# Performance work log

Hardware: AMD Instinct MI355X
Metric: run time of the kernel (lower is better)

Reference implementation:

```python
import jax, jax.numpy as jnp
import numpy as np

N = 8192
NUM_CLASSES = 20
IOU_THRESH = 0.5
IMAGE_SIZE = 1024.0
MAX_DELTA = 16.0


def setup_inputs() -> dict:
    key = jax.random.key(0)
    k1, k2, k3, k4 = jax.random.split(key, 4)
    deltas = jax.random.uniform(k1, (N, 4), dtype=jnp.float32) * MAX_DELTA
    locations = jax.random.uniform(k2, (N, 2), dtype=jnp.float32) * IMAGE_SIZE
    scores = jax.random.uniform(k3, (N,), dtype=jnp.float32)
    class_ids = jax.random.randint(k4, (N,), 0, NUM_CLASSES, dtype=jnp.int32)
    return {"deltas": deltas, "locations": locations, "scores": scores,
            "class_ids": class_ids, "stride": 8}


def _apply_deltas_to_locations(deltas, locations, stride):
    # Faithful to fcos_apply_deltas_to_locations: clamp deltas at 0, then LTRB decode.
    d = jnp.clip(deltas, 0.0, None)
    xc, yc = locations[:, 0], locations[:, 1]
    s = jnp.asarray(stride, deltas.dtype)
    return jnp.stack([xc - d[:, 0] * s,
                      yc - d[:, 1] * s,
                      xc + d[:, 2] * s,
                      yc + d[:, 3] * s], axis=1)  # (N, 4) x1,y1,x2,y2


def _class_spec_nms(boxes, scores, class_ids, iou_threshold):
    # Class-offset trick (same math as class_spec_nms): shift boxes per class so
    # boxes of different classes never overlap.
    max_coord = jnp.max(boxes)
    offsets = class_ids.astype(boxes.dtype) * (max_coord + 1.0)
    b = boxes + offsets[:, None]

    # Sort by descending score (greedy order of the sequential python loop).
    order = jnp.argsort(-scores)
    bs = b[order]
    x1, y1, x2, y2 = bs[:, 0], bs[:, 1], bs[:, 2], bs[:, 3]
    areas = (x2 - x1) * (y2 - y1)

    # Pairwise IoU in sorted order -- the parallel-bitmask form of the
    # sequential suppression (exactly the same IoU math as `nms`).
    xx1 = jnp.maximum(x1[:, None], x1[None, :])
    yy1 = jnp.maximum(y1[:, None], y1[None, :])
    xx2 = jnp.minimum(x2[:, None], x2[None, :])
    yy2 = jnp.minimum(y2[:, None], y2[None, :])
    inter = jnp.clip(xx2 - xx1, 0.0, None) * jnp.clip(yy2 - yy1, 0.0, None)
    union = areas[:, None] + areas[None, :] - inter
    iou = inter / union  # (N, N), no eps, matching the original

    n = boxes.shape[0]
    idx = jnp.arange(n)

    def body(i, keep):
        # Box i suppresses later boxes with IoU > threshold, only if i itself survives.
        sup = keep[i] & (iou[i] > iou_threshold) & (idx > i)
        return keep & ~sup

    keep_sorted = jax.lax.fori_loop(0, n, body, jnp.ones((n,), dtype=bool))
    # Boolean keep mask in ORIGINAL box order (fixed-shape stand-in for the
    # variable-length index list the torch version returns).
    keep_mask = jnp.zeros((n,), dtype=bool).at[order].set(keep_sorted)
    return keep_mask


def reference(deltas, locations, scores, class_ids, stride):
    boxes = _apply_deltas_to_locations(deltas, locations, stride)
    keep_mask = _class_spec_nms(boxes, scores, class_ids, IOU_THRESH)
    return boxes, keep_mask
```

## Files before the change

### kernel.cpp

```cpp
#include <hip/hip_runtime.h>
#include <stdint.h>

#define N 8192
#define NCLS 20
#define IOU_THRESH 0.5f
#define MAXC 576
#define NW 9

typedef unsigned long long u64;

#define WS_BLOCKMAX 0
#define WS_MAXC1    256
#define WS_ORDER    512
#define WS_X1S      33280
#define WS_Y1S      66048
#define WS_X2S      98816
#define WS_Y2S      131584
#define WS_AREAS    164352
#define WS_CLSLIST  197632
#define WS_CLSSTART 230400

__global__ __launch_bounds__(256) void k_boxes(const float* __restrict__ deltas,
                                               const float* __restrict__ loc,
                                               const int* __restrict__ stridep,
                                               float* __restrict__ outBoxes,
                                               float* __restrict__ blockmax) {
    int i = blockIdx.x * blockDim.x + threadIdx.x;
    int iv = stridep[0];
    float sf = (iv >= 0 && iv < (1 << 23)) ? (float)iv : __int_as_float(iv);

    float4 d = ((const float4*)deltas)[i];
    float2 c = ((const float2*)loc)[i];
    float d0 = fmaxf(d.x, 0.0f), d1 = fmaxf(d.y, 0.0f);
    float d2 = fmaxf(d.z, 0.0f), d3 = fmaxf(d.w, 0.0f);
    float p0 = d0 * sf, p1 = d1 * sf, p2 = d2 * sf, p3 = d3 * sf;
    asm volatile("" : "+v"(p0), "+v"(p1), "+v"(p2), "+v"(p3));
    float x1 = c.x - p0, y1 = c.y - p1, x2 = c.x + p2, y2 = c.y + p3;
    float4 b; b.x = x1; b.y = y1; b.z = x2; b.w = y2;
    ((float4*)outBoxes)[i] = b;

    float m = fmaxf(fmaxf(x1, y1), fmaxf(x2, y2));
    for (int off = 32; off; off >>= 1) m = fmaxf(m, __shfl_down(m, off));
    __shared__ float sm[4];
    int wid = threadIdx.x >> 6;
    if ((threadIdx.x & 63) == 0) sm[wid] = m;
    __syncthreads();
    if (threadIdx.x == 0)
        blockmax[blockIdx.x] = fmaxf(fmaxf(sm[0], sm[1]), fmaxf(sm[2], sm[3]));
}

__global__ __launch_bounds__(64) void k_maxreduce(const float* __restrict__ blockmax,
                                                  float* __restrict__ maxc1, int nb) {
    int l = threadIdx.x;
    float m = (l < nb) ? blockmax[l] : -1e38f;
    for (int off = 32; off; off >>= 1) m = fmaxf(m, __shfl_down(m, off));
    if (l == 0) maxc1[0] = m + 1.0f;
}

__global__ __launch_bounds__(1024) void k_sort(const float* __restrict__ scores,
                                               const int* __restrict__ cls,
                                               const float* __restrict__ boxes,
                                               const float* __restrict__ maxc1p,
                                               int* __restrict__ order,
                                               float* __restrict__ x1s, float* __restrict__ y1s,
                                               float* __restrict__ x2s, float* __restrict__ y2s,
                                               float* __restrict__ areas) {
    __shared__ u64 sk[N];
    int t = threadIdx.x;
    for (int m = 0; m < N / 1024; ++m) {
        int i = t + m * 1024;
        unsigned u = __float_as_uint(scores[i]);
        sk[i] = (((u64)(~u)) << 32) | (unsigned)i;
    }
    __syncthreads();
    for (int k = 2; k <= N; k <<= 1) {
        for (int j = k >> 1; j > 0; j >>= 1) {
            for (int m = 0; m < (N / 2) / 1024; ++m) {
                int idx = t + m * 1024;
                int i1 = 2 * idx - (idx & (j - 1));
                int i2 = i1 + j;
                bool dir = ((i1 & k) == 0);
                u64 a = sk[i1], b = sk[i2];
                if ((a > b) == dir) { sk[i1] = b; sk[i2] = a; }
            }
            __syncthreads();
        }
    }
    float mc = maxc1p[0];
    for (int m = 0; m < N / 1024; ++m) {
        int j = t + m * 1024;
        int oi = (int)(sk[j] & 0xFFFFFFFFull);
        order[j] = oi;
        float4 b = ((const float4*)boxes)[oi];
        float off = (float)cls[oi] * mc;
        asm volatile("" : "+v"(off));
        float a1 = b.x + off, a2 = b.y + off, a3 = b.z + off, a4 = b.w + off;
        x1s[j] = a1; y1s[j] = a2; x2s[j] = a3; y2s[j] = a4;
        areas[j] = (a3 - a1) * (a4 - a2);
    }
}

__global__ __launch_bounds__(256) void k_part(const int* __restrict__ order,
                                              const int* __restrict__ cls,
                                              int* __restrict__ clsList,
                                              int* __restrict__ clsStart) {
    __shared__ int cnt[NCLS * 256];
    __shared__ int orig[NCLS * 256];
    __shared__ int part[256];
    int t = threadIdx.x;
    for (int c = 0; c < NCLS; ++c) cnt[c * 256 + t] = 0;
    __syncthreads();
    for (int k = 0; k < 32; ++k) {
        int j = t * 32 + k;
        int c = cls[order[j]];
        cnt[c * 256 + t]++;
    }
    __syncthreads();
    {
        int running = 0;
        for (int k = 0; k < NCLS; ++k) {
            int f = t * NCLS + k;
            int v = cnt[f];
            orig[f] = v;
            running += v;
            cnt[f] = running;
        }
        part[t] = running;
    }
    __syncthreads();
    if (t == 0) {
        int carry = 0;
        for (int u = 0; u < 256; ++u) { int tmp = part[u]; part[u] = carry; carry += tmp; }
    }
    __syncthreads();
    for (int k = 0; k < NCLS; ++k) cnt[t * NCLS + k] += part[t];
    __syncthreads();
    if (t < NCLS) clsStart[t] = cnt[t * 256] - orig[t * 256];
    if (t == NCLS) clsStart[NCLS] = N;
    __syncthreads();
    for (int k = 0; k < NCLS; ++k) { int f = t * NCLS + k; orig[f] = cnt[f] - orig[f]; }
    __syncthreads();
    for (int k = 0; k < 32; ++k) {
        int j = t * 32 + k;
        int c = cls[order[j]];
        int pos = orig[c * 256 + t]++;
        clsList[pos] = j;
    }
}

__global__ __launch_bounds__(256) void k_cnms(const float* __restrict__ x1s, const float* __restrict__ y1s,
                                              const float* __restrict__ x2s, const float* __restrict__ y2s,
                                              const float* __restrict__ areas,
                                              const int* __restrict__ clsList,
                                              const int* __restrict__ clsStart,
                                              const int* __restrict__ order,
                                              float* __restrict__ keep_out) {
    __shared__ float lx1[MAXC], ly1[MAXC], lx2[MAXC], ly2[MAXC], lar[MAXC];
    __shared__ int   lorig[MAXC];
    __shared__ u64   lmask[MAXC][NW];
    __shared__ u64   remv[NW];
    int c = blockIdx.x;
    int s = clsStart[c], e = clsStart[c + 1];
    int n = e - s; if (n > MAXC) n = MAXC;
    int tid = threadIdx.x;
    int nPad = (n + 63) & ~63;
    for (int k = tid; k < nPad; k += 256) {
        if (k < n) {
            int j = clsList[s + k];
            lx1[k] = x1s[j]; ly1[k] = y1s[j]; lx2[k] = x2s[j]; ly2[k] = y2s[j];
            lar[k] = areas[j];
            lorig[k] = order[j];
        } else {
            lx1[k] = -1e30f; ly1[k] = -1e30f; lx2[k] = -1e30f; ly2[k] = -1e30f; lar[k] = 0.f;
        }
        #pragma unroll
        for (int w = 0; w < NW; ++w) lmask[k][w] = 0ull;
    }
    __syncthreads();
    for (int i = tid; i < n; i += 256) {
        float rx1 = lx1[i], ry1 = ly1[i], rx2 = lx2[i], ry2 = ly2[i], rar = lar[i];
        int wEnd = (n - 1) >> 6;
        for (int w = (i >> 6); w <= wEnd; ++w) {
            u64 bits = 0ull;
            int j0 = w << 6;
            #pragma unroll 8
            for (int jj = 0; jj < 64; ++jj) {
                int j = j0 + jj;
                float xx1 = fmaxf(rx1, lx1[j]);
                float yy1 = fmaxf(ry1, ly1[j]);
                float xx2 = fminf(rx2, lx2[j]);
                float yy2 = fminf(ry2, ly2[j]);
                float ww = fmaxf(xx2 - xx1, 0.0f);
                float hh = fmaxf(yy2 - yy1, 0.0f);
                float inter = ww * hh;
                asm volatile("" : "+v"(inter));
                float uni = (rar + lar[j]) - inter;
                float iou = inter / uni;
                bool sup = (iou > IOU_THRESH) && (j > i) && (j < n);
                bits |= ((u64)sup) << jj;
            }
            lmask[i][w] = bits;
        }
    }
    __syncthreads();
    if (tid < 64) {
        int lane = tid;
        u64 r = 0ull;
        u64 nextrow = (lane < NW && n > 0) ? lmask[0][lane] : 0ull;
        for (int i = 0; i < n; ++i) {
            u64 row = nextrow;
            nextrow = (lane < NW && i + 1 < n) ? lmask[i + 1][lane] : 0ull;
            bool bit = (lane == (i >> 6)) && ((r >> (i & 63)) & 1ull);
            u64 kmask = __any(bit ? 1 : 0) ? 0ull : ~0ull;
            r |= row & kmask;
        }
        if (lane < NW) remv[lane] = r;
    }
    __syncthreads();
    for (int k = tid; k < n; k += 256) {
        u64 w = remv[k >> 6];
        keep_out[lorig[k]] = ((w >> (k & 63)) & 1ull) ? 0.0f : 1.0f;
    }
}

extern "C" void kernel_launch(void* const* d_in, const int* in_sizes, int n_in,
                              void* d_out, int out_size, void* d_ws, size_t ws_size,
                              hipStream_t stream) {
    const float* deltas  = (const float*)d_in[0];
    const float* loc     = (const float*)d_in[1];
    const float* scores  = (const float*)d_in[2];
    const int*   cls     = (const int*)d_in[3];
    const int*   stridep = (const int*)d_in[4];
    float* out = (float*)d_out;

    char* ws = (char*)d_ws;
    float* blockmax = (float*)(ws + WS_BLOCKMAX);
    float* maxc1    = (float*)(ws + WS_MAXC1);
    int*   order    = (int*)(ws + WS_ORDER);
    float* x1s      = (float*)(ws + WS_X1S);
    float* y1s      = (float*)(ws + WS_Y1S);
    float* x2s      = (float*)(ws + WS_X2S);
    float* y2s      = (float*)(ws + WS_Y2S);
    float* areas    = (float*)(ws + WS_AREAS);
    int*   clsList  = (int*)(ws + WS_CLSLIST);
    int*   clsStart = (int*)(ws + WS_CLSSTART);

    k_boxes<<<N / 256, 256, 0, stream>>>(deltas, loc, stridep, out, blockmax);
    k_maxreduce<<<1, 64, 0, stream>>>(blockmax, maxc1, N / 256);
    k_sort<<<1, 1024, 0, stream>>>(scores, cls, out, maxc1, order, x1s, y1s, x2s, y2s, areas);
    k_part<<<1, 256, 0, stream>>>(order, cls, clsList, clsStart);
    k_cnms<<<NCLS, 256, 0, stream>>>(x1s, y1s, x2s, y2s, areas, clsList, clsStart, order, out + 4 * N);
}
```

Baseline: 260.7 us.

## Resolve NMS suppression per 64-box block with diagonal readlane scan

Replaces the per-row serial suppression loop, which did a wave vote for every box, with a block-wise scheme. For each 64-box block, the diagonal mask word is held per lane, and the surviving boxes inside the block are resolved with scalar readlane and ctz iteration. Only the rows of the kept boxes are then OR-ed into the running removal mask, in batches of 8 LDS loads. This cuts the serial dependency chain and skips loading rows of suppressed boxes, at the cost of more complex control flow.

Result: no change. 257.2 us (-1.4%).

```diff
diff --git a/kernel.cpp b/kernel.cpp
--- a/kernel.cpp
+++ b/kernel.cpp
@@ -206,13 +206,42 @@
     if (tid < 64) {
         int lane = tid;
         u64 r = 0ull;
-        u64 nextrow = (lane < NW && n > 0) ? lmask[0][lane] : 0ull;
-        for (int i = 0; i < n; ++i) {
-            u64 row = nextrow;
-            nextrow = (lane < NW && i + 1 < n) ? lmask[i + 1][lane] : 0ull;
-            bool bit = (lane == (i >> 6)) && ((r >> (i & 63)) & 1ull);
-            u64 kmask = __any(bit ? 1 : 0) ? 0ull : ~0ull;
-            r |= row & kmask;
+        int nblk = (n + 63) >> 6;
+        u64 dg = (nblk > 0) ? lmask[lane][0] : 0ull;
+        for (int b = 0; b < nblk; ++b) {
+            unsigned rlo = (unsigned)r, rhi = (unsigned)(r >> 32);
+            u64 pre = ((u64)(unsigned)__builtin_amdgcn_readlane((int)rhi, b) << 32)
+                    |  (u64)(unsigned)__builtin_amdgcn_readlane((int)rlo, b);
+            unsigned dlo = (unsigned)dg, dhi = (unsigned)(dg >> 32);
+            u64 sup = pre;
+            u64 alive = ~pre;
+            u64 km = 0ull;
+            while (alive) {
+                int i = __builtin_ctzll(alive);
+                km |= (1ull << i);
+                u64 row = ((u64)(unsigned)__builtin_amdgcn_readlane((int)dhi, i) << 32)
+                        |  (u64)(unsigned)__builtin_amdgcn_readlane((int)dlo, i);
+                sup |= row;
+                alive &= ~(sup | (1ull << i));
+            }
+            u64 dg_next = (b + 1 < nblk) ? lmask[64 * (b + 1) + lane][b + 1] : 0ull;
+            u64 kk = km;
+            while (kk) {
+                u64 vals[8];
+                #pragma unroll
+                for (int g = 0; g < 8; ++g) {
+                    u64 v = 0ull;
+                    if (kk) {
+                        int j = __builtin_ctzll(kk);
+                        kk &= kk - 1;
+                        if (lane < NW) v = lmask[64 * b + j][lane];
+                    }
+                    vals[g] = v;
+                }
+                #pragma unroll
+                for (int g = 0; g < 8; ++g) r |= vals[g];
+            }
+            dg = dg_next;
         }
         if (lane < NW) remv[lane] = r;
     }
```
